# Optimization experiments

Measured on AMD Instinct MI355X. Metric: run time of the kernel, lower is better.

Reference implementation:

```python
import jax, jax.numpy as jnp
import numpy as np

N_NODES = 100000
N_EDGES = 1600000
IN_DIM = 768
HIDDEN = 256
N_CLASSES = 3


def setup_inputs() -> dict:
    key = jax.random.key(0)
    k0, k1, k2, k3 = jax.random.split(key, 4)
    x = jax.random.normal(k0, (N_NODES, IN_DIM), dtype=jnp.float32)
    edge_index = jax.random.randint(k1, (2, N_EDGES), 0, N_NODES, dtype=jnp.int32)
    # Glorot-ish init for weights
    W1 = jax.random.normal(k2, (IN_DIM, HIDDEN), dtype=jnp.float32) * (1.0 / np.sqrt(IN_DIM))
    b1 = jnp.zeros((HIDDEN,), dtype=jnp.float32)
    W2 = jax.random.normal(k3, (HIDDEN, N_CLASSES), dtype=jnp.float32) * (1.0 / np.sqrt(HIDDEN))
    b2 = jnp.zeros((N_CLASSES,), dtype=jnp.float32)
    return {"x": x, "edge_index": edge_index, "W1": W1, "b1": b1, "W2": W2, "b2": b2}


def reference(x, edge_index, W1, b1, W2, b2):
    """dumb_GNN forward: GCNConv(768->H) -> relu -> (dropout=eval identity) -> Linear -> log_softmax.

    GCNConv math (PyG default): out = D^{-1/2} (A + I) D^{-1/2} X W + b
    """
    n = x.shape[0]
    src, dst = edge_index[0], edge_index[1]
    # add self-loops
    loops = jnp.arange(n, dtype=src.dtype)
    src = jnp.concatenate([src, loops])
    dst = jnp.concatenate([dst, loops])
    # symmetric degree normalization (degrees include self-loops)
    deg = jax.ops.segment_sum(jnp.ones_like(src, dtype=x.dtype), dst, num_segments=n)
    dinv = jnp.where(deg > 0, jax.lax.rsqrt(deg), jnp.zeros_like(deg))
    norm = dinv[src] * dinv[dst]  # [E+N]
    # transform then gather-scale-scatter aggregate
    h = x @ W1  # [N, H]
    agg = jax.ops.segment_sum(h[src] * norm[:, None], dst, num_segments=n) + b1
    h = jax.nn.relu(agg)
    # dropout is identity at inference
    logits = h @ W2 + b2  # [N, C]
    return jax.nn.log_softmax(logits, axis=-1)
```

## Files before the change

### kernel.cpp

```cpp
#include <hip/hip_runtime.h>
#include <hip/hip_bf16.h>
#include <math.h>

#define N_NODES 100000
#define N_EDGES 1600000
#define IN_DIM  768
#define HIDDEN  256

#define SCAN_B  256
#define N_SBLK  ((N_NODES + SCAN_B - 1) / SCAN_B)

#define H_OFF    0ull
#define ADJ_OFF  51200000ull
#define RS_OFF   57600000ull
#define CUR_OFF  58000016ull
#define DEG_OFF  58400016ull
#define DINV_OFF 58800016ull
#define W1T_OFF  59200016ull
#define BSUM_OFF 59593232ull

typedef short          bf16x8 __attribute__((ext_vector_type(8)));
typedef float          fp32x4 __attribute__((ext_vector_type(4)));
typedef float          fp32x8 __attribute__((ext_vector_type(8)));
typedef unsigned short u16x8  __attribute__((ext_vector_type(8)));

__device__ inline short f2bf(float f) {
    union { float f; unsigned u; } c; c.f = f;
    unsigned u = c.u;
    unsigned r = u + 0x7FFFu + ((u >> 16) & 1u);
    return (short)(r >> 16);
}

__device__ inline fp32x8 bf8_to_f8(u16x8 v) {
    fp32x8 r;
    for (int j = 0; j < 8; j++) {
        union { unsigned u; float f; } c;
        c.u = ((unsigned)v[j]) << 16;
        r[j] = c.f;
    }
    return r;
}

__device__ inline void gl_lds16(const short* g, short* l) {
    __builtin_amdgcn_global_load_lds(
        (const __attribute__((address_space(1))) unsigned int*)g,
        (__attribute__((address_space(3))) unsigned int*)l, 16, 0, 0);
}

__global__ void init_kernel(int* __restrict__ deg, int* __restrict__ cursor) {
    int i = blockIdx.x * blockDim.x + threadIdx.x;
    if (i < N_NODES) { deg[i] = 0; cursor[i] = 0; }
}

__global__ void w1t_kernel(const float* __restrict__ w1, short* __restrict__ w1t) {
    int i = blockIdx.x * blockDim.x + threadIdx.x;
    if (i < HIDDEN * IN_DIM) {
        int n = i / IN_DIM, k = i % IN_DIM;
        w1t[i] = f2bf(w1[(size_t)k * HIDDEN + n]);
    }
}

__global__ void count_kernel(const int* __restrict__ dst, int* __restrict__ deg) {
    int e = blockIdx.x * blockDim.x + threadIdx.x;
    if (e < N_EDGES) atomicAdd(&deg[dst[e]], 1);
}

__global__ __launch_bounds__(SCAN_B) void scan1_kernel(const int* __restrict__ deg,
                                                       int* __restrict__ bsum) {
    int i = blockIdx.x * SCAN_B + threadIdx.x;
    int v = (i < N_NODES) ? deg[i] : 0;
    for (int off = 32; off > 0; off >>= 1) v += __shfl_down(v, off, 64);
    __shared__ int wsum[SCAN_B / 64];
    int lane = threadIdx.x & 63, w = threadIdx.x >> 6;
    if (lane == 0) wsum[w] = v;
    __syncthreads();
    if (threadIdx.x == 0) {
        int s = 0;
        for (int j = 0; j < SCAN_B / 64; j++) s += wsum[j];
        bsum[blockIdx.x] = s;
    }
}

__global__ __launch_bounds__(512) void scan2_kernel(int* __restrict__ bsum) {
    __shared__ int s[512];
    int tid = threadIdx.x;
    int v = (tid < N_SBLK) ? bsum[tid] : 0;
    s[tid] = v;
    __syncthreads();
    for (int off = 1; off < 512; off <<= 1) {
        int t = (tid >= off) ? s[tid - off] : 0;
        __syncthreads();
        s[tid] += t;
        __syncthreads();
    }
    if (tid < N_SBLK) bsum[tid] = s[tid] - v;
}

__global__ __launch_bounds__(SCAN_B) void scan3_kernel(const int* __restrict__ deg,
                                                       const int* __restrict__ bsum,
                                                       int* __restrict__ row_start,
                                                       float* __restrict__ dinv) {
    __shared__ int s[SCAN_B];
    int i = blockIdx.x * SCAN_B + threadIdx.x;
    int tid = threadIdx.x;
    int d = (i < N_NODES) ? deg[i] : 0;
    s[tid] = d;
    __syncthreads();
    for (int off = 1; off < SCAN_B; off <<= 1) {
        int t = (tid >= off) ? s[tid - off] : 0;
        __syncthreads();
        s[tid] += t;
        __syncthreads();
    }
    if (i < N_NODES) {
        row_start[i] = bsum[blockIdx.x] + s[tid] - d;
        dinv[i] = rsqrtf((float)(d + 1));
        if (i == N_NODES - 1) row_start[N_NODES] = N_EDGES;
    }
}

__global__ void fill_kernel(const int* __restrict__ src, const int* __restrict__ dst,
                            const int* __restrict__ row_start, int* __restrict__ cursor,
                            int* __restrict__ adj) {
    int e = blockIdx.x * blockDim.x + threadIdx.x;
    if (e < N_EDGES) {
        int d = dst[e];
        int p = row_start[d] + atomicAdd(&cursor[d], 1);
        adj[p] = src[e];
    }
}

__global__ __launch_bounds__(256) void gemm1_kernel(const float* __restrict__ x,
                                                    const short* __restrict__ w1t,
                                                    const float* __restrict__ dinv,
                                                    unsigned short* __restrict__ h) {
    __shared__ __attribute__((aligned(16))) short a_lds[2][4096];
    __shared__ __attribute__((aligned(16))) short b_lds[2][4096];

    const int tid  = threadIdx.x;
    const int lane = tid & 63;
    const int wave = tid >> 6;
    const int wm = (wave >> 1) * 64;
    const int wn = (wave & 1) * 64;
    const int l15 = lane & 15;
    const int q   = lane >> 4;
    const int row0 = blockIdx.x * 128;
    const int col0 = blockIdx.y * 128;

    const int arow = tid & 127;
    const int aq   = (tid >> 7) * 2;
    const int agr  = row0 + arow;
    const bool aok = agr < N_NODES;
    const float* axp = x + (size_t)agr * IN_DIM + aq * 8;

    const int bslot0 = wave * 64 + lane;
    const int bslot1 = 256 + wave * 64 + lane;
    const short* bgp0 = w1t + (size_t)(col0 + (bslot0 & 127)) * IN_DIM + (bslot0 >> 7) * 8;
    const short* bgp1 = w1t + (size_t)(col0 + (bslot1 & 127)) * IN_DIM + (bslot1 >> 7) * 8;
    short* const bl0base0 = &b_lds[0][(size_t)(wave * 64) * 8];
    short* const bl0base1 = &b_lds[0][(size_t)(256 + wave * 64) * 8];
    short* const bl1base0 = &b_lds[1][(size_t)(wave * 64) * 8];
    short* const bl1base1 = &b_lds[1][(size_t)(256 + wave * 64) * 8];

    fp32x4 acc[4][4];
    for (int i = 0; i < 4; i++)
        for (int j = 0; j < 4; j++)
            for (int r = 0; r < 4; r++) acc[i][j][r] = 0.0f;

    gl_lds16(bgp0, bl0base0);
    gl_lds16(bgp1, bl0base1);
    {
        fp32x4 p0 = {0,0,0,0}, p1 = {0,0,0,0}, p2 = {0,0,0,0}, p3 = {0,0,0,0};
        if (aok) {
            p0 = *(const fp32x4*)axp;       p1 = *(const fp32x4*)(axp + 4);
            p2 = *(const fp32x4*)(axp + 8); p3 = *(const fp32x4*)(axp + 12);
        }
        bf16x8 av;
        av[0]=f2bf(p0[0]); av[1]=f2bf(p0[1]); av[2]=f2bf(p0[2]); av[3]=f2bf(p0[3]);
        av[4]=f2bf(p1[0]); av[5]=f2bf(p1[1]); av[6]=f2bf(p1[2]); av[7]=f2bf(p1[3]);
        *(bf16x8*)(&a_lds[0][(size_t)(aq * 128 + arow) * 8]) = av;
        av[0]=f2bf(p2[0]); av[1]=f2bf(p2[1]); av[2]=f2bf(p2[2]); av[3]=f2bf(p2[3]);
        av[4]=f2bf(p3[0]); av[5]=f2bf(p3[1]); av[6]=f2bf(p3[2]); av[7]=f2bf(p3[3]);
        *(bf16x8*)(&a_lds[0][(size_t)((aq + 1) * 128 + arow) * 8]) = av;
    }

    int cur = 0;
    for (int k0 = 0; k0 < IN_DIM; k0 += 32) {
        __syncthreads();
        const int nxt = cur ^ 1;
        const bool more = (k0 + 32) < IN_DIM;

        fp32x4 p0, p1, p2, p3;
        if (more) {
            gl_lds16(bgp0 + k0 + 32, nxt ? bl1base0 : bl0base0);
            gl_lds16(bgp1 + k0 + 32, nxt ? bl1base1 : bl0base1);
            if (aok) {
                const float* p = axp + k0 + 32;
                p0 = *(const fp32x4*)p;       p1 = *(const fp32x4*)(p + 4);
                p2 = *(const fp32x4*)(p + 8); p3 = *(const fp32x4*)(p + 12);
            } else {
                p0 = p1 = p2 = p3 = (fp32x4){0,0,0,0};
            }
        }

        bf16x8 af[4], bfr[4];
        for (int mt = 0; mt < 4; mt++)
            af[mt] = *(const bf16x8*)(&a_lds[cur][(size_t)(q * 128 + wm + mt * 16 + l15) * 8]);
        for (int nt = 0; nt < 4; nt++)
            bfr[nt] = *(const bf16x8*)(&b_lds[cur][(size_t)(q * 128 + wn + nt * 16 + l15) * 8]);
        for (int mt = 0; mt < 4; mt++)
            for (int nt = 0; nt < 4; nt++)
                acc[mt][nt] = __builtin_amdgcn_mfma_f32_16x16x32_bf16(
                    af[mt], bfr[nt], acc[mt][nt], 0, 0, 0);

        if (more) {
            bf16x8 av;
            av[0]=f2bf(p0[0]); av[1]=f2bf(p0[1]); av[2]=f2bf(p0[2]); av[3]=f2bf(p0[3]);
            av[4]=f2bf(p1[0]); av[5]=f2bf(p1[1]); av[6]=f2bf(p1[2]); av[7]=f2bf(p1[3]);
            *(bf16x8*)(&a_lds[nxt][(size_t)(aq * 128 + arow) * 8]) = av;
            av[0]=f2bf(p2[0]); av[1]=f2bf(p2[1]); av[2]=f2bf(p2[2]); av[3]=f2bf(p2[3]);
            av[4]=f2bf(p3[0]); av[5]=f2bf(p3[1]); av[6]=f2bf(p3[2]); av[7]=f2bf(p3[3]);
            *(bf16x8*)(&a_lds[nxt][(size_t)((aq + 1) * 128 + arow) * 8]) = av;
        }
        cur = nxt;
    }

    float dv[4][4];
    for (int mt = 0; mt < 4; mt++)
        for (int r = 0; r < 4; r++) {
            int row = row0 + wm + mt * 16 + q * 4 + r;
            dv[mt][r] = (row < N_NODES) ? dinv[row] : 0.0f;
        }
    for (int mt = 0; mt < 4; mt++) {
        for (int nt = 0; nt < 4; nt++) {
            int col = col0 + wn + nt * 16 + l15;
            for (int r = 0; r < 4; r++) {
                int row = row0 + wm + mt * 16 + q * 4 + r;
                if (row < N_NODES)
                    h[(size_t)row * HIDDEN + col] =
                        (unsigned short)f2bf(dv[mt][r] * acc[mt][nt][r]);
            }
        }
    }
}

__global__ __launch_bounds__(256) void aggregate_kernel(
    const unsigned short* __restrict__ h, const int* __restrict__ adj,
    const int* __restrict__ row_start, const float* __restrict__ dinv,
    const float* __restrict__ b1, const float* __restrict__ w2,
    const float* __restrict__ b2, float* __restrict__ out) {
    const int lane = threadIdx.x & 63;
    const int wave = threadIdx.x >> 6;
    const int half = lane >> 5;
    const int l32  = lane & 31;
    const int v = blockIdx.x * 8 + wave * 2 + half;

    const size_t choff = (size_t)l32 * 8;

    fp32x8 a0 = bf8_to_f8(*(const u16x8*)(h + (size_t)v * HIDDEN + choff));
    fp32x8 a1 = {0,0,0,0,0,0,0,0}, a2 = a1, a3 = a1;

    int e0 = row_start[v], e1 = row_start[v + 1];
    for (int e = e0; e < e1; e += 32) {
        int cnt = min(32, e1 - e);
        int s = (l32 < cnt) ? adj[e + l32] : 0;
        int i = 0;
        for (; i + 4 <= cnt; i += 4) {
            int s0 = __shfl(s, i,     32);
            int s1 = __shfl(s, i + 1, 32);
            int s2 = __shfl(s, i + 2, 32);
            int s3 = __shfl(s, i + 3, 32);
            u16x8 r0 = *(const u16x8*)(h + (size_t)s0 * HIDDEN + choff);
            u16x8 r1 = *(const u16x8*)(h + (size_t)s1 * HIDDEN + choff);
            u16x8 r2 = *(const u16x8*)(h + (size_t)s2 * HIDDEN + choff);
            u16x8 r3 = *(const u16x8*)(h + (size_t)s3 * HIDDEN + choff);
            a0 += bf8_to_f8(r0);
            a1 += bf8_to_f8(r1);
            a2 += bf8_to_f8(r2);
            a3 += bf8_to_f8(r3);
        }
        for (; i < cnt; i++) {
            int si = __shfl(s, i, 32);
            a0 += bf8_to_f8(*(const u16x8*)(h + (size_t)si * HIDDEN + choff));
        }
    }
    fp32x8 acc = (a0 + a1) + (a2 + a3);

    float dvv = dinv[v];
    float hr[8];
    for (int j = 0; j < 8; j++)
        hr[j] = fmaxf(0.0f, dvv * acc[j] + b1[choff + j]);

    float p0 = 0.f, p1 = 0.f, p2 = 0.f;
    for (int j = 0; j < 8; j++) {
        const float* wr = w2 + (choff + j) * 3;
        p0 += hr[j] * wr[0];
        p1 += hr[j] * wr[1];
        p2 += hr[j] * wr[2];
    }
    for (int off = 16; off > 0; off >>= 1) {
        p0 += __shfl_down(p0, off, 32);
        p1 += __shfl_down(p1, off, 32);
        p2 += __shfl_down(p2, off, 32);
    }
    if (l32 == 0) {
        p0 += b2[0]; p1 += b2[1]; p2 += b2[2];
        float m = fmaxf(p0, fmaxf(p1, p2));
        float l = logf(expf(p0 - m) + expf(p1 - m) + expf(p2 - m));
        out[(size_t)v * 3 + 0] = p0 - m - l;
        out[(size_t)v * 3 + 1] = p1 - m - l;
        out[(size_t)v * 3 + 2] = p2 - m - l;
    }
}

extern "C" void kernel_launch(void* const* d_in, const int* in_sizes, int n_in,
                              void* d_out, int out_size, void* d_ws, size_t ws_size,
                              hipStream_t stream) {
    const float* x    = (const float*)d_in[0];
    const int*   ei   = (const int*)d_in[1];
    const float* W1   = (const float*)d_in[2];
    const float* b1   = (const float*)d_in[3];
    const float* W2   = (const float*)d_in[4];
    const float* b2   = (const float*)d_in[5];
    float* out = (float*)d_out;

    const int* src = ei;
    const int* dst = ei + N_EDGES;

    char* ws = (char*)d_ws;
    unsigned short* h_ws = (unsigned short*)(ws + H_OFF);
    int*   adj       = (int*)(ws + ADJ_OFF);
    int*   row_start = (int*)(ws + RS_OFF);
    int*   cursor    = (int*)(ws + CUR_OFF);
    int*   deg       = (int*)(ws + DEG_OFF);
    float* dinv      = (float*)(ws + DINV_OFF);
    short* w1t       = (short*)(ws + W1T_OFF);
    int*   bsum      = (int*)(ws + BSUM_OFF);

    init_kernel<<<(N_NODES + 255) / 256, 256, 0, stream>>>(deg, cursor);
    w1t_kernel<<<(HIDDEN * IN_DIM + 255) / 256, 256, 0, stream>>>(W1, w1t);
    count_kernel<<<(N_EDGES + 255) / 256, 256, 0, stream>>>(dst, deg);
    scan1_kernel<<<N_SBLK, SCAN_B, 0, stream>>>(deg, bsum);
    scan2_kernel<<<1, 512, 0, stream>>>(bsum);
    scan3_kernel<<<N_SBLK, SCAN_B, 0, stream>>>(deg, bsum, row_start, dinv);
    fill_kernel<<<(N_EDGES + 255) / 256, 256, 0, stream>>>(src, dst, row_start, cursor, adj);
    gemm1_kernel<<<dim3((N_NODES + 127) / 128, HIDDEN / 128), 256, 0, stream>>>(x, w1t, dinv, h_ws);
    aggregate_kernel<<<N_NODES / 8, 256, 0, stream>>>(h_ws, adj, row_start, dinv, b1, W2, b2, out);
}
```

Baseline: 826.4 us.

## Single-buffer GEMM1 LDS with register prefetch and packed bf16 conversion

Restructures the X·W1 GEMM main loop. LDS double buffering and the direct global-to-LDS loads for W1 are dropped in favour of a single LDS buffer. The next K-slice of both A and B is prefetched into registers while the current one runs on MFMA. Scalar bf16 rounding is replaced by packed float2-to-bfloat162 conversion. This halves LDS use, which may raise occupancy, but it adds a second barrier per iteration and drops the direct-to-LDS path.

Measured after the change: 823.2 us. No clear change (-0.4%).

```diff
diff --git a/kernel.cpp b/kernel.cpp
--- a/kernel.cpp
+++ b/kernel.cpp
@@ -31,6 +31,22 @@
     return (short)(r >> 16);
 }
 
+__device__ inline unsigned pk2(float x, float y) {
+    __hip_bfloat162 h = __float22bfloat162_rn(make_float2(x, y));
+    union { __hip_bfloat162 h2; unsigned u; } c;
+    c.h2 = h;
+    return c.u;
+}
+
+__device__ inline bf16x8 cvt8(fp32x4 a, fp32x4 b) {
+    union { bf16x8 v; unsigned u[4]; } r;
+    r.u[0] = pk2(a[0], a[1]);
+    r.u[1] = pk2(a[2], a[3]);
+    r.u[2] = pk2(b[0], b[1]);
+    r.u[3] = pk2(b[2], b[3]);
+    return r.v;
+}
+
 __device__ inline fp32x8 bf8_to_f8(u16x8 v) {
     fp32x8 r;
     for (int j = 0; j < 8; j++) {
@@ -39,12 +55,6 @@
         r[j] = c.f;
     }
     return r;
-}
-
-__device__ inline void gl_lds16(const short* g, short* l) {
-    __builtin_amdgcn_global_load_lds(
-        (const __attribute__((address_space(1))) unsigned int*)g,
-        (__attribute__((address_space(3))) unsigned int*)l, 16, 0, 0);
 }
 
 __global__ void init_kernel(int* __restrict__ deg, int* __restrict__ cursor) {
@@ -134,8 +144,8 @@
                                                     const short* __restrict__ w1t,
                                                     const float* __restrict__ dinv,
                                                     unsigned short* __restrict__ h) {
-    __shared__ __attribute__((aligned(16))) short a_lds[2][4096];
-    __shared__ __attribute__((aligned(16))) short b_lds[2][4096];
+    __shared__ __attribute__((aligned(16))) short a_lds[4096];
+    __shared__ __attribute__((aligned(16))) short b_lds[4096];
 
     const int tid  = threadIdx.x;
     const int lane = tid & 63;
@@ -157,72 +167,48 @@
     const int bslot1 = 256 + wave * 64 + lane;
     const short* bgp0 = w1t + (size_t)(col0 + (bslot0 & 127)) * IN_DIM + (bslot0 >> 7) * 8;
     const short* bgp1 = w1t + (size_t)(col0 + (bslot1 & 127)) * IN_DIM + (bslot1 >> 7) * 8;
-    short* const bl0base0 = &b_lds[0][(size_t)(wave * 64) * 8];
-    short* const bl0base1 = &b_lds[0][(size_t)(256 + wave * 64) * 8];
-    short* const bl1base0 = &b_lds[1][(size_t)(wave * 64) * 8];
-    short* const bl1base1 = &b_lds[1][(size_t)(256 + wave * 64) * 8];
 
     fp32x4 acc[4][4];
     for (int i = 0; i < 4; i++)
         for (int j = 0; j < 4; j++)
             for (int r = 0; r < 4; r++) acc[i][j][r] = 0.0f;
 
-    gl_lds16(bgp0, bl0base0);
-    gl_lds16(bgp1, bl0base1);
-    {
-        fp32x4 p0 = {0,0,0,0}, p1 = {0,0,0,0}, p2 = {0,0,0,0}, p3 = {0,0,0,0};
-        if (aok) {
-            p0 = *(const fp32x4*)axp;       p1 = *(const fp32x4*)(axp + 4);
-            p2 = *(const fp32x4*)(axp + 8); p3 = *(const fp32x4*)(axp + 12);
-        }
-        bf16x8 av;
-        av[0]=f2bf(p0[0]); av[1]=f2bf(p0[1]); av[2]=f2bf(p0[2]); av[3]=f2bf(p0[3]);
-        av[4]=f2bf(p1[0]); av[5]=f2bf(p1[1]); av[6]=f2bf(p1[2]); av[7]=f2bf(p1[3]);
-        *(bf16x8*)(&a_lds[0][(size_t)(aq * 128 + arow) * 8]) = av;
-        av[0]=f2bf(p2[0]); av[1]=f2bf(p2[1]); av[2]=f2bf(p2[2]); av[3]=f2bf(p2[3]);
-        av[4]=f2bf(p3[0]); av[5]=f2bf(p3[1]); av[6]=f2bf(p3[2]); av[7]=f2bf(p3[3]);
-        *(bf16x8*)(&a_lds[0][(size_t)((aq + 1) * 128 + arow) * 8]) = av;
-    }
-
-    int cur = 0;
+    fp32x4 p0 = {0,0,0,0}, p1 = {0,0,0,0}, p2 = {0,0,0,0}, p3 = {0,0,0,0};
+    if (aok) {
+        p0 = *(const fp32x4*)axp;       p1 = *(const fp32x4*)(axp + 4);
+        p2 = *(const fp32x4*)(axp + 8); p3 = *(const fp32x4*)(axp + 12);
+    }
+    bf16x8 pb0 = *(const bf16x8*)bgp0;
+    bf16x8 pb1 = *(const bf16x8*)bgp1;
+
     for (int k0 = 0; k0 < IN_DIM; k0 += 32) {
-        __syncthreads();
-        const int nxt = cur ^ 1;
-        const bool more = (k0 + 32) < IN_DIM;
-
-        fp32x4 p0, p1, p2, p3;
-        if (more) {
-            gl_lds16(bgp0 + k0 + 32, nxt ? bl1base0 : bl0base0);
-            gl_lds16(bgp1 + k0 + 32, nxt ? bl1base1 : bl0base1);
+        *(bf16x8*)(&a_lds[(size_t)(aq * 128 + arow) * 8])       = cvt8(p0, p1);
+        *(bf16x8*)(&a_lds[(size_t)((aq + 1) * 128 + arow) * 8]) = cvt8(p2, p3);
+        *(bf16x8*)(&b_lds[(size_t)bslot0 * 8]) = pb0;
+        *(bf16x8*)(&b_lds[(size_t)bslot1 * 8]) = pb1;
+        __syncthreads();
+
+        int kn = k0 + 32;
+        if (kn < IN_DIM) {
             if (aok) {
-                const float* p = axp + k0 + 32;
+                const float* p = axp + kn;
                 p0 = *(const fp32x4*)p;       p1 = *(const fp32x4*)(p + 4);
                 p2 = *(const fp32x4*)(p + 8); p3 = *(const fp32x4*)(p + 12);
-            } else {
-                p0 = p1 = p2 = p3 = (fp32x4){0,0,0,0};
             }
+            pb0 = *(const bf16x8*)(bgp0 + kn);
+            pb1 = *(const bf16x8*)(bgp1 + kn);
         }
 
         bf16x8 af[4], bfr[4];
         for (int mt = 0; mt < 4; mt++)
-            af[mt] = *(const bf16x8*)(&a_lds[cur][(size_t)(q * 128 + wm + mt * 16 + l15) * 8]);
+            af[mt] = *(const bf16x8*)(&a_lds[(size_t)(q * 128 + wm + mt * 16 + l15) * 8]);
         for (int nt = 0; nt < 4; nt++)
-            bfr[nt] = *(const bf16x8*)(&b_lds[cur][(size_t)(q * 128 + wn + nt * 16 + l15) * 8]);
+            bfr[nt] = *(const bf16x8*)(&b_lds[(size_t)(q * 128 + wn + nt * 16 + l15) * 8]);
         for (int mt = 0; mt < 4; mt++)
             for (int nt = 0; nt < 4; nt++)
                 acc[mt][nt] = __builtin_amdgcn_mfma_f32_16x16x32_bf16(
                     af[mt], bfr[nt], acc[mt][nt], 0, 0, 0);
-
-        if (more) {
-            bf16x8 av;
-            av[0]=f2bf(p0[0]); av[1]=f2bf(p0[1]); av[2]=f2bf(p0[2]); av[3]=f2bf(p0[3]);
-            av[4]=f2bf(p1[0]); av[5]=f2bf(p1[1]); av[6]=f2bf(p1[2]); av[7]=f2bf(p1[3]);
-            *(bf16x8*)(&a_lds[nxt][(size_t)(aq * 128 + arow) * 8]) = av;
-            av[0]=f2bf(p2[0]); av[1]=f2bf(p2[1]); av[2]=f2bf(p2[2]); av[3]=f2bf(p2[3]);
-            av[4]=f2bf(p3[0]); av[5]=f2bf(p3[1]); av[6]=f2bf(p3[2]); av[7]=f2bf(p3[3]);
-            *(bf16x8*)(&a_lds[nxt][(size_t)((aq + 1) * 128 + arow) * 8]) = av;
-        }
-        cur = nxt;
+        __syncthreads();
     }
 
     float dv[4][4];
```
